# Kernel optimization log

Hardware: AMD Instinct MI355X
Metric: run time of the kernel (lower is better)

## Reference

```python
import itertools
import jax, jax.numpy as jnp
import numpy as np


def setup_inputs() -> dict:
    key = jax.random.key(0)
    k1, k2 = jax.random.split(key)
    B, N, D = 32, 32, 16          # batch, n_objects, rel_dim
    F, K = 16, 3                  # n_filters, kernel_size
    R = jax.random.normal(k1, (B, N, N, D), dtype=jnp.float32)
    filters = jax.random.normal(k2, (F, K, K, D), dtype=jnp.float32)
    return {"R": R, "filters": filters}


def reference(R, filters):
    # R: (B, n_objects, n_objects, rel_dim); filters: (n_filters, k, k, rel_dim)
    B, n_objects, _, rel_dim = R.shape
    k = filters.shape[1]
    # groups_type='combinations': all size-k index combinations (static, shape (G, k))
    groups = jnp.asarray(
        list(itertools.combinations(range(n_objects), k)), dtype=jnp.int32
    )
    # Vectorized per-group double gather: (B, G, k, k, rel_dim)
    R_sub = R[:, groups[:, :, None], groups[:, None, :], :]
    # Relational inner product against all filters: sum over (i, j, d)
    # -> (B, n_groups, n_filters)
    return jnp.einsum("bgijd,fijd->bgf", R_sub, filters)
```

## Files before the change

kernel.cpp:

```cpp
#include <hip/hip_runtime.h>
#include <stdint.h>


#define NOBJ 32
#define NG   4960
#define NF   16
#define ND   16

typedef __bf16 bf16x8 __attribute__((ext_vector_type(8)));
typedef float  f32x4  __attribute__((ext_vector_type(4)));

__device__ __forceinline__ unsigned f2bf1(float x) {
    unsigned u = __float_as_uint(x);
    return (u + 0x7fffu + ((u >> 16) & 1u)) >> 16;
}
__device__ __forceinline__ unsigned packbf(float lo, float hi) {
    return f2bf1(lo) | (f2bf1(hi) << 16);
}
__device__ __forceinline__ bf16x8 pack8(float4 a, float4 b) {
    union { unsigned u[4]; bf16x8 v; } r;
    r.u[0] = packbf(a.x, a.y); r.u[1] = packbf(a.z, a.w);
    r.u[2] = packbf(b.x, b.y); r.u[3] = packbf(b.z, b.w);
    return r.v;
}

__device__ __forceinline__ int C3i(int x) { return (x * (x - 1) * (x - 2)) / 6; }
__device__ __forceinline__ int C2i(int x) { return (x * (x - 1)) >> 1; }

__device__ __forceinline__ void unrank3_cf(int g, int& t0, int& t1, int& t2) {
    const int T = 4960 - g;
    int x = (int)cbrtf(6.0f * (float)T) + 1;
    x += (C3i(x) < T);
    x += (C3i(x) < T);
    x -= (C3i(x - 1) >= T);
    x -= (C3i(x - 1) >= T);
    t0 = 32 - x;
    const int rem2 = C3i(x) - T;
    const int T2   = C2i(x - 1) - rem2;
    int y = (int)(sqrtf(2.0f * (float)T2) + 0.5f);
    y += (C2i(y) < T2);
    y += (C2i(y) < T2);
    y -= (C2i(y - 1) >= T2);
    y -= (C2i(y - 1) >= T2);
    t1 = 32 - y;
    t2 = t1 + 1 + (C2i(y) - T2);
}

__global__ __launch_bounds__(256) void rgc_fused(
    const float* __restrict__ R,
    const float* __restrict__ Fw,
    float* __restrict__ out)
{
    const int tid  = threadIdx.x;
    const int wave = tid >> 6;
    const int lane = tid & 63;
    const int l15  = lane & 15;
    const int quad = lane >> 4;
    const int b0   = blockIdx.y * 2;
    const int gw   = blockIdx.x * 64 + wave * 16;

    const int g = min(gw + l15, NG - 1);
    int t0, t1, t2;
    unrank3_cf(g, t0, t1, t2);
    const int t[3] = {t0, t1, t2};

    int rowoff[9];
#pragma unroll
    for (int ij = 0; ij < 9; ++ij) {
        const int i = ij / 3, j = ij % 3;
        rowoff[ij] = (t[i] * NOBJ + t[j]) * ND;
    }

    const int hi = quad >> 1;
    const int d0 = (quad & 1) * 8;
    int ro[5];
    ro[0] = hi ? rowoff[1] : rowoff[0];
    ro[1] = hi ? rowoff[3] : rowoff[2];
    ro[2] = hi ? rowoff[5] : rowoff[4];
    ro[3] = hi ? rowoff[7] : rowoff[6];
    ro[4] = rowoff[8];

    bf16x8 wf[5];
#pragma unroll
    for (int s = 0; s < 5; ++s) {
        const int ksafe = (s < 4) ? (s * 32 + quad * 8) : (128 + (quad & 1) * 8);
        const float4* wp = (const float4*)(Fw + l15 * 144 + ksafe);
        bf16x8 w = pack8(wp[0], wp[1]);
        if (s == 4 && quad >= 2) w = (bf16x8)(__bf16)0.0f;
        wf[s] = w;
    }

    const int gbase = gw + quad * 4;
#pragma unroll
    for (int bb = 0; bb < 2; ++bb) {
        const int b = b0 + bb;
        const float* Rb = R + (size_t)b * (NOBJ * NOBJ * ND);
        f32x4 acc = {0.f, 0.f, 0.f, 0.f};
#pragma unroll
        for (int s = 0; s < 5; ++s) {
            const float4* ap = (const float4*)(Rb + ro[s] + d0);
            const bf16x8 a = pack8(ap[0], ap[1]);
            acc = __builtin_amdgcn_mfma_f32_16x16x32_bf16(a, wf[s], acc, 0, 0, 0);
        }
#pragma unroll
        for (int r = 0; r < 4; ++r) {
            const int gg = gbase + r;
            if (gg < NG) out[((size_t)b * NG + gg) * NF + l15] = acc[r];
        }
    }
}

extern "C" void kernel_launch(void* const* d_in, const int* in_sizes, int n_in,
                              void* d_out, int out_size, void* d_ws, size_t ws_size,
                              hipStream_t stream) {
    const float* R  = (const float*)d_in[0];
    const float* Fw = (const float*)d_in[1];
    if (n_in >= 2 && in_sizes[0] == NF * 9 * ND) { R = (const float*)d_in[1]; Fw = (const float*)d_in[0]; }
    float* out = (float*)d_out;
    dim3 grid((NG + 63) / 64, 16);
    rgc_fused<<<grid, dim3(256, 1, 1), 0, stream>>>(R, Fw, out);
}
```

Baseline: 67.26 us.

## Stage per-batch R slice as bf16 in LDS and gather groups from shared memory

Each block now handles one batch and 128 groups. It first converts that batch's whole 32x32x16 R slice to bf16 and stores it in shared memory (32 KB), then has each wave loop over 16-group tiles, gathering MFMA A operands from LDS instead of re-reading and converting global fp32 rows. This removes redundant scattered global loads and repeated conversions across overlapping combinations. The cost is that every block reloads the full slice (39 blocks per batch), which adds global traffic and sync latency, and the 32 KB of LDS per block limits occupancy.

```diff
diff --git a/kernel.cpp b/kernel.cpp
--- a/kernel.cpp
+++ b/kernel.cpp
@@ -6,6 +6,7 @@
 #define NG   4960
 #define NF   16
 #define ND   16
+#define SLICE (NOBJ * NOBJ * ND)
 
 typedef __bf16 bf16x8 __attribute__((ext_vector_type(8)));
 typedef float  f32x4  __attribute__((ext_vector_type(4)));
@@ -51,34 +52,28 @@
     const float* __restrict__ Fw,
     float* __restrict__ out)
 {
+    __shared__ unsigned short sA[SLICE];
+
     const int tid  = threadIdx.x;
     const int wave = tid >> 6;
     const int lane = tid & 63;
     const int l15  = lane & 15;
     const int quad = lane >> 4;
-    const int b0   = blockIdx.y * 2;
-    const int gw   = blockIdx.x * 64 + wave * 16;
+    const int b    = blockIdx.y;
+    const int g0   = blockIdx.x * 128;
+    const int ngt  = min(8, (NG >> 4) - blockIdx.x * 8);
 
-    const int g = min(gw + l15, NG - 1);
-    int t0, t1, t2;
-    unrank3_cf(g, t0, t1, t2);
-    const int t[3] = {t0, t1, t2};
-
-    int rowoff[9];
+    const float* Rb = R + (size_t)b * SLICE;
 #pragma unroll
-    for (int ij = 0; ij < 9; ++ij) {
-        const int i = ij / 3, j = ij % 3;
-        rowoff[ij] = (t[i] * NOBJ + t[j]) * ND;
+    for (int k = 0; k < 8; ++k) {
+        const int e = (tid + k * 256) * 8;
+        const float4 p0 = *(const float4*)(Rb + e);
+        const float4 p1 = *(const float4*)(Rb + e + 4);
+        union { unsigned u[4]; uint4 v; } r;
+        r.u[0] = packbf(p0.x, p0.y); r.u[1] = packbf(p0.z, p0.w);
+        r.u[2] = packbf(p1.x, p1.y); r.u[3] = packbf(p1.z, p1.w);
+        *(uint4*)&sA[e] = r.v;
     }
-
-    const int hi = quad >> 1;
-    const int d0 = (quad & 1) * 8;
-    int ro[5];
-    ro[0] = hi ? rowoff[1] : rowoff[0];
-    ro[1] = hi ? rowoff[3] : rowoff[2];
-    ro[2] = hi ? rowoff[5] : rowoff[4];
-    ro[3] = hi ? rowoff[7] : rowoff[6];
-    ro[4] = rowoff[8];
 
     bf16x8 wf[5];
 #pragma unroll
@@ -90,23 +85,40 @@
         wf[s] = w;
     }
 
-    const int gbase = gw + quad * 4;
+    __syncthreads();
+
+    const int hi = quad >> 1;
+    const int d0 = (quad & 1) * 8;
+
+    for (int gt = wave; gt < ngt; gt += 4) {
+        const int g = g0 + gt * 16 + l15;
+        int t0, t1, t2;
+        unrank3_cf(g, t0, t1, t2);
+        const int t[3] = {t0, t1, t2};
+
+        int rowoff[9];
 #pragma unroll
-    for (int bb = 0; bb < 2; ++bb) {
-        const int b = b0 + bb;
-        const float* Rb = R + (size_t)b * (NOBJ * NOBJ * ND);
+        for (int ij = 0; ij < 9; ++ij) {
+            const int i = ij / 3, j = ij % 3;
+            rowoff[ij] = (t[i] * NOBJ + t[j]) * ND;
+        }
+        int ro[5];
+        ro[0] = hi ? rowoff[1] : rowoff[0];
+        ro[1] = hi ? rowoff[3] : rowoff[2];
+        ro[2] = hi ? rowoff[5] : rowoff[4];
+        ro[3] = hi ? rowoff[7] : rowoff[6];
+        ro[4] = rowoff[8];
+
         f32x4 acc = {0.f, 0.f, 0.f, 0.f};
 #pragma unroll
         for (int s = 0; s < 5; ++s) {
-            const float4* ap = (const float4*)(Rb + ro[s] + d0);
-            const bf16x8 a = pack8(ap[0], ap[1]);
+            const bf16x8 a = *(const bf16x8*)&sA[ro[s] + d0];
             acc = __builtin_amdgcn_mfma_f32_16x16x32_bf16(a, wf[s], acc, 0, 0, 0);
         }
+
+        const size_t obase = ((size_t)b * NG + g0 + gt * 16 + quad * 4) * NF + l15;
 #pragma unroll
-        for (int r = 0; r < 4; ++r) {
-            const int gg = gbase + r;
-            if (gg < NG) out[((size_t)b * NG + gg) * NF + l15] = acc[r];
-        }
+        for (int r = 0; r < 4; ++r) out[obase + (size_t)r * NF] = acc[r];
     }
 }
 
@@ -117,6 +129,6 @@
     const float* Fw = (const float*)d_in[1];
     if (n_in >= 2 && in_sizes[0] == NF * 9 * ND) { R = (const float*)d_in[1]; Fw = (const float*)d_in[0]; }
     float* out = (float*)d_out;
-    dim3 grid((NG + 63) / 64, 16);
+    dim3 grid(39, 32);
     rgc_fused<<<grid, dim3(256, 1, 1), 0, stream>>>(R, Fw, out);
 }
```

Result: no change. 67.25 us (-0.0%).
